# Optimization experiments

Hardware: AMD Instinct MI355X
Metric: run time of the kernel (lower is better)

## Reference

```python
import jax, jax.numpy as jnp
import numpy as np

DELTA = 1.0


def _l2_normalize(x, eps=0.0):
    # matches torch x / x.norm(p=2, dim=-1, keepdim=True)
    return x / jnp.linalg.norm(x, axis=-1, keepdims=True)


def _cosine_rows(a, b):
    # row-wise cosine similarity of matching rows: [N, D] x [N, D] -> [N]
    return jnp.sum(_l2_normalize(a) * _l2_normalize(b), axis=-1)


def setup_inputs() -> dict:
    key = jax.random.key(0)
    kq, kt = jax.random.split(key)
    N, D = 16384, 128
    queries = jax.random.normal(kq, (N, D), dtype=jnp.float32)
    targets = jax.random.normal(kt, (N, D), dtype=jnp.float32)
    return {"queries": queries, "targets": targets}


def reference(queries, targets):
    N = targets.shape[0]
    # ---- hard-negative mining (torch does this under no_grad) ----
    # torch builds an [N, N, D] broadcast then reduces; we fuse it as a
    # normalized GEMM producing the [N, N] cosine-sim matrix directly.
    bn = _l2_normalize(targets)                      # [N, D]
    sim = bn @ bn.T                                   # [N, N] cosine sims
    sim = sim - jnp.eye(N, dtype=sim.dtype)           # knock out the diagonal
    idx = jnp.argmax(sim, axis=0)                     # hardest negative per col
    wrong = targets[idx]                              # [N, D]
    # ---- hinge loss ----
    pos = _cosine_rows(queries, targets)              # [N]
    neg = _cosine_rows(queries, wrong)                # [N]
    return jnp.mean(jax.nn.relu(DELTA - pos + neg))
```

## Files before the change

### kernel.cpp

```cpp
#include <hip/hip_runtime.h>
#include <hip/hip_bf16.h>

#define N 16384
#define D 128
#define RS 16
#define CT 32
#define ROWS_PER_SPLIT (N / RS)
#define ITERS (ROWS_PER_SPLIT / 32)

typedef __attribute__((ext_vector_type(4))) int i32x4;
typedef __attribute__((ext_vector_type(16))) int i32x16;

__global__ __launch_bounds__(256) void knorm(const float* __restrict__ t,
                                             char* __restrict__ bnq) {
    const int row  = blockIdx.x * 4 + (threadIdx.x >> 6);
    const int lane = threadIdx.x & 63;
    const float2 v = *(const float2*)(t + (size_t)row * D + lane * 2);
    float ss = v.x * v.x + v.y * v.y;
#pragma unroll
    for (int m = 1; m <= 32; m <<= 1) ss += __shfl_xor(ss, m, 64);
    const float inv = rsqrtf(ss) * 127.0f;
    char2 o;
    o.x = (char)__float2int_rn(v.x * inv);
    o.y = (char)__float2int_rn(v.y * inv);
    *(char2*)(bnq + (size_t)row * 128 + lane * 2) = o;
}

__global__ __launch_bounds__(256, 2) void kargmax(const char* __restrict__ bnq,
                                                  int* __restrict__ pval,
                                                  int* __restrict__ pcode) {
    const int tid  = threadIdx.x;
    const int lane = tid & 63;
    const int w    = tid >> 6;
    const int b    = blockIdx.x;
    const int s    = (b & 7) * 2 + ((b >> 3) & 1);
    const int ct   = b >> 4;
    const int j0w  = ct * 512 + w * 128;
    const int rbase = s * ROWS_PER_SPLIT;

    const int cl = lane & 31;
    const int hi = lane >> 5;
    const int rloc = cl - 4 * hi;

    i32x4 fb[4][4];
#pragma unroll
    for (int c4 = 0; c4 < 4; ++c4)
#pragma unroll
        for (int ks = 0; ks < 4; ++ks)
            fb[c4][ks] = *(const i32x4*)(bnq + (size_t)(j0w + c4 * 32 + cl) * 128 +
                                         ks * 32 + hi * 16);

    const char* aptr = bnq + (size_t)(rbase + cl) * 128 + hi * 16;

    int mv[4];
#pragma unroll
    for (int c4 = 0; c4 < 4; ++c4) mv[c4] = INT_MIN;
    int gb = hi;

    const i32x16 z16 = {0,0,0,0,0,0,0,0,0,0,0,0,0,0,0,0};
    i32x4 fA[4], fB[4];

#define LOADF(buf, itv) do {                                  \
    const char* p_ = aptr + (size_t)(itv) * 4096;             \
    buf[0] = *(const i32x4*)(p_);                             \
    buf[1] = *(const i32x4*)(p_ + 32);                        \
    buf[2] = *(const i32x4*)(p_ + 64);                        \
    buf[3] = *(const i32x4*)(p_ + 96); } while (0)

#define COMPUTEF(buf, itv) do {                                                             \
    const int r0_ = rbase + (itv) * 32;                                                     \
    const bool dg_ = ((unsigned)(r0_ - j0w) < 128u);                                        \
    i32x16 acc[4];                                                                          \
    __builtin_amdgcn_s_setprio(1);                                                          \
    _Pragma("unroll")                                                                       \
    for (int c4 = 0; c4 < 4; ++c4)                                                          \
        acc[c4] = __builtin_amdgcn_mfma_i32_32x32x32_i8(buf[0], fb[c4][0], z16, 0, 0, 0);   \
    _Pragma("unroll")                                                                       \
    for (int ks = 1; ks < 4; ++ks) {                                                        \
        _Pragma("unroll")                                                                   \
        for (int c4 = 0; c4 < 4; ++c4)                                                      \
            acc[c4] = __builtin_amdgcn_mfma_i32_32x32x32_i8(buf[ks], fb[c4][ks],            \
                                                            acc[c4], 0, 0, 0);              \
    }                                                                                       \
    __builtin_amdgcn_s_setprio(0);                                                          \
    if (dg_) {                                                                              \
        _Pragma("unroll")                                                                   \
        for (int c4 = 0; c4 < 4; ++c4)                                                      \
            if (r0_ == j0w + c4 * 32) {                                                     \
                _Pragma("unroll")                                                           \
                for (int r = 0; r < 16; ++r)                                                \
                    if (rloc == ((r & 3) + 8 * (r >> 2))) acc[c4][r] -= (1 << 30);          \
            }                                                                               \
    }                                                                                       \
    _Pragma("unroll")                                                                       \
    for (int c4 = 0; c4 < 4; ++c4) {                                                        \
        _Pragma("unroll")                                                                   \
        for (int g = 0; g < 4; ++g) {                                                       \
            const int m_ = max(max(acc[c4][4*g], acc[c4][4*g+1]),                           \
                               max(acc[c4][4*g+2], acc[c4][4*g+3]));                        \
            const int p_ = (int)(((unsigned)m_ << 8)) + (gb + 2 * g);                       \
            mv[c4] = max(mv[c4], p_);                                                       \
        }                                                                                   \
    }                                                                                       \
    gb += 8; } while (0)

    LOADF(fA, 0);
    LOADF(fB, 1);
    for (int it2 = 0; it2 < ITERS; it2 += 2) {
        COMPUTEF(fA, it2);     LOADF(fA, it2 + 2);
        COMPUTEF(fB, it2 + 1); LOADF(fB, it2 + 3);
    }
#undef LOADF
#undef COMPUTEF

#pragma unroll
    for (int c4 = 0; c4 < 4; ++c4) {
        int v = mv[c4];
        v = max(v, __shfl_xor(v, 32, 64));
        if (lane < 32) {
            pval[(size_t)s * N + j0w + c4 * 32 + cl]  = v;
            pcode[(size_t)s * N + j0w + c4 * 32 + cl] = rbase + (v & 255) * 4;
        }
    }
}

__global__ __launch_bounds__(256) void kloss(const float* __restrict__ q,
                                             const float* __restrict__ t,
                                             const int* __restrict__ pval,
                                             const int* __restrict__ pcode,
                                             float* __restrict__ bsum) {
    const int j    = blockIdx.x * 4 + (threadIdx.x >> 6);
    const int lane = threadIdx.x & 63;

    int v = INT_MIN;
    int c = 0;
    if (lane < RS) { v = pval[(size_t)lane * N + j]; c = pcode[(size_t)lane * N + j]; }
#pragma unroll
    for (int m = 1; m <= 8; m <<= 1) {
        const int ov = __shfl_xor(v, m, 64);
        const int oc = __shfl_xor(c, m, 64);
        if (ov > v || (ov == v && oc < c)) { v = ov; c = oc; }
    }
    c = __shfl(c, 0, 64);

    const float2 qv = *(const float2*)(q + (size_t)j * D + lane * 2);
    const float2 tv = *(const float2*)(t + (size_t)j * D + lane * 2);
    float qq = qv.x * qv.x + qv.y * qv.y;
    float tt = tv.x * tv.x + tv.y * tv.y;
    float qt = qv.x * tv.x + qv.y * tv.y;
    float ww[4], wt[4], qw[4];
#pragma unroll
    for (int r = 0; r < 4; ++r) {
        const float2 wv = *(const float2*)(t + (size_t)(c + r) * D + lane * 2);
        ww[r] = wv.x * wv.x + wv.y * wv.y;
        wt[r] = wv.x * tv.x + wv.y * tv.y;
        qw[r] = wv.x * qv.x + wv.y * qv.y;
    }
#pragma unroll
    for (int m = 1; m <= 32; m <<= 1) {
        qq += __shfl_xor(qq, m, 64);
        tt += __shfl_xor(tt, m, 64);
        qt += __shfl_xor(qt, m, 64);
#pragma unroll
        for (int r = 0; r < 4; ++r) {
            ww[r] += __shfl_xor(ww[r], m, 64);
            wt[r] += __shfl_xor(wt[r], m, 64);
            qw[r] += __shfl_xor(qw[r], m, 64);
        }
    }
    const float pos = qt * rsqrtf(qq * tt);
    float best = -1e30f, neg = 0.f;
#pragma unroll
    for (int r = 0; r < 4; ++r) {
        float cr = wt[r] * rsqrtf(ww[r] * tt);
        if (c + r == j) cr -= 1.0f;
        if (cr > best) { best = cr; neg = qw[r] * rsqrtf(qq * ww[r]); }
    }
    const float l = fmaxf(0.f, 1.0f - pos + neg);

    __shared__ float ls[4];
    if (lane == 0) ls[threadIdx.x >> 6] = l;
    __syncthreads();
    if (threadIdx.x == 0) bsum[blockIdx.x] = ls[0] + ls[1] + ls[2] + ls[3];
}

__global__ __launch_bounds__(256) void kfinal(const float* __restrict__ bsum,
                                              float* __restrict__ out) {
    float sum = 0.f;
    for (int i = threadIdx.x; i < N / 4; i += 256) sum += bsum[i];
#pragma unroll
    for (int m = 1; m <= 32; m <<= 1) sum += __shfl_xor(sum, m, 64);
    __shared__ float ws2[4];
    if ((threadIdx.x & 63) == 0) ws2[threadIdx.x >> 6] = sum;
    __syncthreads();
    if (threadIdx.x == 0) out[0] = (ws2[0] + ws2[1] + ws2[2] + ws2[3]) * (1.0f / N);
}

extern "C" void kernel_launch(void* const* d_in, const int* in_sizes, int n_in,
                              void* d_out, int out_size, void* d_ws, size_t ws_size,
                              hipStream_t stream) {
    const float* q = (const float*)d_in[0];
    const float* t = (const float*)d_in[1];
    char* ws = (char*)d_ws;

    char* bnq = ws;
    int*  pval = (int*)(ws + (size_t)N * 128);
    int*  pcode = (int*)(ws + (size_t)N * 128 + (size_t)RS * N * 4);
    float* bsum = (float*)(ws + (size_t)N * 128 + (size_t)2 * RS * N * 4);

    knorm<<<dim3(N / 4), dim3(256), 0, stream>>>(t, bnq);
    kargmax<<<dim3(CT * RS), dim3(256), 0, stream>>>(bnq, pval, pcode);
    kloss<<<dim3(N / 4), dim3(256), 0, stream>>>(q, t, pval, pcode, bsum);
    kfinal<<<dim3(1), dim3(256), 0, stream>>>(bsum, (float*)d_out);
}
```

Measured before the change: 71.15 us.

## Switch argmax GEMM to 16x16x64 int8 MFMA with smaller column tiles

The argmax kernel now uses the 16x16x64 int8 MFMA instead of 32x32x32. Each wave covers 64 columns instead of 128, so the grid of column tiles doubles, and the register footprint shrinks enough to raise launch bounds occupancy to 4 blocks per CU. Accumulators drop from 16 to 4 per tile, which simplifies the max packing and diagonal masking. The trade-off is more A-row reloads per output, since each row tile is reused over fewer columns, and one extra shuffle in the final reduction.

Result: slower. 97.60 us (+37.2%).

```diff
diff --git a/kernel.cpp b/kernel.cpp
--- a/kernel.cpp
+++ b/kernel.cpp
@@ -4,12 +4,11 @@
 #define N 16384
 #define D 128
 #define RS 16
-#define CT 32
+#define CT 64
 #define ROWS_PER_SPLIT (N / RS)
-#define ITERS (ROWS_PER_SPLIT / 32)
+#define ITERS (ROWS_PER_SPLIT / 16)
 
 typedef __attribute__((ext_vector_type(4))) int i32x4;
-typedef __attribute__((ext_vector_type(16))) int i32x16;
 
 __global__ __launch_bounds__(256) void knorm(const float* __restrict__ t,
                                              char* __restrict__ bnq) {
@@ -26,83 +25,72 @@
     *(char2*)(bnq + (size_t)row * 128 + lane * 2) = o;
 }
 
-__global__ __launch_bounds__(256, 2) void kargmax(const char* __restrict__ bnq,
+__global__ __launch_bounds__(256, 4) void kargmax(const char* __restrict__ bnq,
                                                   int* __restrict__ pval,
                                                   int* __restrict__ pcode) {
     const int tid  = threadIdx.x;
     const int lane = tid & 63;
     const int w    = tid >> 6;
     const int b    = blockIdx.x;
-    const int s    = (b & 7) * 2 + ((b >> 3) & 1);
-    const int ct   = b >> 4;
-    const int j0w  = ct * 512 + w * 128;
+    const int x    = b & 7;
+    const int i    = b >> 3;
+    const int s    = x * 2 + (i & 1);
+    const int ct   = i >> 1;
+    const int j0w  = ct * 256 + w * 64;
     const int rbase = s * ROWS_PER_SPLIT;
 
-    const int cl = lane & 31;
-    const int hi = lane >> 5;
-    const int rloc = cl - 4 * hi;
-
-    i32x4 fb[4][4];
+    const int lr = lane & 15;
+    const int lk = lane >> 4;
+
+    i32x4 fb[4][2];
 #pragma unroll
     for (int c4 = 0; c4 < 4; ++c4)
 #pragma unroll
-        for (int ks = 0; ks < 4; ++ks)
-            fb[c4][ks] = *(const i32x4*)(bnq + (size_t)(j0w + c4 * 32 + cl) * 128 +
-                                         ks * 32 + hi * 16);
-
-    const char* aptr = bnq + (size_t)(rbase + cl) * 128 + hi * 16;
+        for (int ks = 0; ks < 2; ++ks)
+            fb[c4][ks] = *(const i32x4*)(bnq + (size_t)(j0w + c4 * 16 + lr) * 128 +
+                                         ks * 64 + lk * 16);
+
+    const char* aptr = bnq + (size_t)(rbase + lr) * 128 + lk * 16;
 
     int mv[4];
 #pragma unroll
     for (int c4 = 0; c4 < 4; ++c4) mv[c4] = INT_MIN;
-    int gb = hi;
-
-    const i32x16 z16 = {0,0,0,0,0,0,0,0,0,0,0,0,0,0,0,0};
-    i32x4 fA[4], fB[4];
+    int gb = lk;
+
+    const i32x4 z4 = {0, 0, 0, 0};
+    i32x4 fA[2], fB[2];
 
 #define LOADF(buf, itv) do {                                  \
-    const char* p_ = aptr + (size_t)(itv) * 4096;             \
+    const char* p_ = aptr + (size_t)(itv) * 2048;             \
     buf[0] = *(const i32x4*)(p_);                             \
-    buf[1] = *(const i32x4*)(p_ + 32);                        \
-    buf[2] = *(const i32x4*)(p_ + 64);                        \
-    buf[3] = *(const i32x4*)(p_ + 96); } while (0)
+    buf[1] = *(const i32x4*)(p_ + 64); } while (0)
 
 #define COMPUTEF(buf, itv) do {                                                             \
-    const int r0_ = rbase + (itv) * 32;                                                     \
-    const bool dg_ = ((unsigned)(r0_ - j0w) < 128u);                                        \
-    i32x16 acc[4];                                                                          \
+    const int r0_ = rbase + (itv) * 16;                                                     \
+    i32x4 acc[4];                                                                           \
     __builtin_amdgcn_s_setprio(1);                                                          \
     _Pragma("unroll")                                                                       \
     for (int c4 = 0; c4 < 4; ++c4)                                                          \
-        acc[c4] = __builtin_amdgcn_mfma_i32_32x32x32_i8(buf[0], fb[c4][0], z16, 0, 0, 0);   \
+        acc[c4] = __builtin_amdgcn_mfma_i32_16x16x64_i8(buf[0], fb[c4][0], z4, 0, 0, 0);    \
     _Pragma("unroll")                                                                       \
-    for (int ks = 1; ks < 4; ++ks) {                                                        \
+    for (int c4 = 0; c4 < 4; ++c4)                                                          \
+        acc[c4] = __builtin_amdgcn_mfma_i32_16x16x64_i8(buf[1], fb[c4][1], acc[c4], 0, 0, 0); \
+    __builtin_amdgcn_s_setprio(0);                                                          \
+    if ((unsigned)(r0_ - j0w) < 64u) {                                                      \
         _Pragma("unroll")                                                                   \
         for (int c4 = 0; c4 < 4; ++c4)                                                      \
-            acc[c4] = __builtin_amdgcn_mfma_i32_32x32x32_i8(buf[ks], fb[c4][ks],            \
-                                                            acc[c4], 0, 0, 0);              \
-    }                                                                                       \
-    __builtin_amdgcn_s_setprio(0);                                                          \
-    if (dg_) {                                                                              \
-        _Pragma("unroll")                                                                   \
-        for (int c4 = 0; c4 < 4; ++c4)                                                      \
-            if (r0_ == j0w + c4 * 32) {                                                     \
+            if (r0_ == j0w + c4 * 16) {                                                     \
                 _Pragma("unroll")                                                           \
-                for (int r = 0; r < 16; ++r)                                                \
-                    if (rloc == ((r & 3) + 8 * (r >> 2))) acc[c4][r] -= (1 << 30);          \
+                for (int r = 0; r < 4; ++r)                                                 \
+                    if (lk * 4 + r == lr) acc[c4][r] -= (1 << 30);                          \
             }                                                                               \
     }                                                                                       \
     _Pragma("unroll")                                                                       \
     for (int c4 = 0; c4 < 4; ++c4) {                                                        \
-        _Pragma("unroll")                                                                   \
-        for (int g = 0; g < 4; ++g) {                                                       \
-            const int m_ = max(max(acc[c4][4*g], acc[c4][4*g+1]),                           \
-                               max(acc[c4][4*g+2], acc[c4][4*g+3]));                        \
-            const int p_ = (int)(((unsigned)m_ << 8)) + (gb + 2 * g);                       \
-            mv[c4] = max(mv[c4], p_);                                                       \
-        }                                                                                   \
+        const int m_ = max(max(acc[c4][0], acc[c4][1]), max(acc[c4][2], acc[c4][3]));       \
+        mv[c4] = max(mv[c4], (int)(((unsigned)m_ << 8)) + gb);                              \
     }                                                                                       \
-    gb += 8; } while (0)
+    gb += 4; } while (0)
 
     LOADF(fA, 0);
     LOADF(fB, 1);
@@ -116,10 +104,11 @@
 #pragma unroll
     for (int c4 = 0; c4 < 4; ++c4) {
         int v = mv[c4];
+        v = max(v, __shfl_xor(v, 16, 64));
         v = max(v, __shfl_xor(v, 32, 64));
-        if (lane < 32) {
-            pval[(size_t)s * N + j0w + c4 * 32 + cl]  = v;
-            pcode[(size_t)s * N + j0w + c4 * 32 + cl] = rbase + (v & 255) * 4;
+        if (lane < 16) {
+            pval[(size_t)s * N + j0w + c4 * 16 + lr]  = v;
+            pcode[(size_t)s * N + j0w + c4 * 16 + lr] = rbase + (v & 255) * 4;
         }
     }
 }
```
